# Kernel optimization log

Measured on AMD Instinct MI355X. Metric: run time of the kernel, lower is better.

Reference implementation:

```python
import jax, jax.numpy as jnp
import numpy as np

N_NODES = 100000
N_EDGES = 1600000
F_IN = 128
HID = 128
N_CLASSES = 32
N_GRAPHS = 512


def _seg_mean(vals, idx, num_segments):
    s = jax.ops.segment_sum(vals, idx, num_segments=num_segments)
    cnt = jax.ops.segment_sum(jnp.ones((vals.shape[0],), vals.dtype), idx, num_segments=num_segments)
    return s / jnp.maximum(cnt, 1.0)[:, None]


def _sage_conv(x, src, dst, Wl, bl, Wr):
    # PyG SAGEConv(mean): out = lin_l(mean_{j in N(i)} x_j) + lin_r(x_i); lin_l has bias, lin_r does not.
    agg = _seg_mean(x[src], dst, N_NODES)          # gather + scatter-mean  [N, d]
    return agg @ Wl.T + bl + x @ Wr.T              # [N, H]


def setup_inputs() -> dict:
    key = jax.random.key(0)
    ks = jax.random.split(key, 16)
    x = jax.random.normal(ks[0], (N_NODES, F_IN), dtype=jnp.float32)
    edge_index = jax.random.randint(ks[1], (2, N_EDGES), 0, N_NODES, dtype=jnp.int64)
    batch = jnp.sort(jax.random.randint(ks[2], (N_NODES,), 0, N_GRAPHS, dtype=jnp.int64))
    sc = 0.05
    params = {
        'Wl0': jax.random.normal(ks[3], (HID, F_IN), jnp.float32) * sc,
        'bl0': jnp.zeros((HID,), jnp.float32),
        'Wr0': jax.random.normal(ks[4], (HID, F_IN), jnp.float32) * sc,
        'Wl1': jax.random.normal(ks[5], (HID, HID), jnp.float32) * sc,
        'bl1': jnp.zeros((HID,), jnp.float32),
        'Wr1': jax.random.normal(ks[6], (HID, HID), jnp.float32) * sc,
        'Wl2': jax.random.normal(ks[7], (HID, HID), jnp.float32) * sc,
        'bl2': jnp.zeros((HID,), jnp.float32),
        'Wr2': jax.random.normal(ks[8], (HID, HID), jnp.float32) * sc,
        'Wlin': jax.random.normal(ks[9], (N_CLASSES, HID), jnp.float32) * sc,
        'blin': jnp.zeros((N_CLASSES,), jnp.float32),
    }
    return {'x': x, 'edge_index': edge_index, 'batch': batch, **params}


def reference(x, edge_index, batch, Wl0, bl0, Wr0, Wl1, bl1, Wr1, Wl2, bl2, Wr2, Wlin, blin):
    src, dst = edge_index[0], edge_index[1]
    # GraphSAGE backbone: relu between layers, no act after last (out_channels set); dropout=identity in eval.
    h = jax.nn.relu(_sage_conv(x, src, dst, Wl0, bl0, Wr0))
    h = jax.nn.relu(_sage_conv(h, src, dst, Wl1, bl1, Wr1))
    h = _sage_conv(h, src, dst, Wl2, bl2, Wr2)
    # global_mean_pool over batch index -> [n_graphs, HID]
    g = _seg_mean(h, batch, N_GRAPHS)
    return g @ Wlin.T + blin  # [n_graphs, n_classes]
```

## Files before the change

kernel.cpp:

```cpp
#include <hip/hip_runtime.h>
#include <hip/hip_bf16.h>


typedef __attribute__((ext_vector_type(8))) short short8v;
typedef __attribute__((ext_vector_type(4))) float f32x4;

#define RK_CH 12544
#define RK_NS 64

__device__ __forceinline__ unsigned short f2bf(float f) {
    __hip_bfloat16 h = __float2bfloat16(f);
    return *reinterpret_cast<unsigned short*>(&h);
}
__device__ __forceinline__ float bf_lo(unsigned u) { return __uint_as_float(u << 16); }
__device__ __forceinline__ float bf_hi(unsigned u) { return __uint_as_float(u & 0xffff0000u); }
__device__ __forceinline__ unsigned packbf(float lo, float hi) {
    return ((unsigned)f2bf(hi) << 16) | f2bf(lo);
}


__launch_bounds__(256)
__global__ void rank_hist_kernel(const int* __restrict__ dst,
                                 unsigned short* __restrict__ rank16,
                                 unsigned short* __restrict__ counts16,
                                 int nE, int nChunk, int es) {
    __shared__ unsigned cnt[RK_CH];
    int s = blockIdx.x / nChunk;
    int c = blockIdx.x % nChunk;
    int lo = c * RK_CH;
    for (int i = threadIdx.x; i < RK_CH; i += 256) cnt[i] = 0u;
    __syncthreads();

    int ebeg = s * es;
    int eend = ebeg + es; if (eend > nE) eend = nE;

    if (ebeg < eend) {
        if ((((size_t)dst) & 15) == 0) {
            int nvec = (eend - ebeg) >> 2;
            for (int g = threadIdx.x; g < nvec; g += 256) {
                int e = ebeg + g * 4;
                int4 d4 = *(const int4*)&dst[e];
                unsigned dc;
                dc = (unsigned)(d4.x - lo);
                if (dc < RK_CH) rank16[e]     = (unsigned short)atomicAdd(&cnt[dc], 1u);
                dc = (unsigned)(d4.y - lo);
                if (dc < RK_CH) rank16[e + 1] = (unsigned short)atomicAdd(&cnt[dc], 1u);
                dc = (unsigned)(d4.z - lo);
                if (dc < RK_CH) rank16[e + 2] = (unsigned short)atomicAdd(&cnt[dc], 1u);
                dc = (unsigned)(d4.w - lo);
                if (dc < RK_CH) rank16[e + 3] = (unsigned short)atomicAdd(&cnt[dc], 1u);
            }
            for (int e = ebeg + (nvec << 2) + threadIdx.x; e < eend; e += 256) {
                unsigned dc = (unsigned)(dst[e] - lo);
                if (dc < RK_CH) rank16[e] = (unsigned short)atomicAdd(&cnt[dc], 1u);
            }
        } else {
            for (int e = ebeg + threadIdx.x; e < eend; e += 256) {
                unsigned dc = (unsigned)(dst[e] - lo);
                if (dc < RK_CH) rank16[e] = (unsigned short)atomicAdd(&cnt[dc], 1u);
            }
        }
    }
    __syncthreads();
    size_t base = ((size_t)(c * RK_NS + s)) * RK_CH;
    for (int i = threadIdx.x; i < RK_CH; i += 256)
        counts16[base + i] = (unsigned short)cnt[i];
}

__global__ void seg_offsets_kernel(unsigned short* __restrict__ counts16,
                                   int* __restrict__ deg, int n) {
    int d = blockIdx.x * blockDim.x + threadIdx.x;
    if (d >= n) return;
    int c = d / RK_CH;
    int i = d - c * RK_CH;
    size_t base = ((size_t)c * RK_NS) * RK_CH + i;
    unsigned run = 0;
    for (int s = 0; s < RK_NS; ++s) {
        size_t idx = base + (size_t)s * RK_CH;
        unsigned v = counts16[idx];
        counts16[idx] = (unsigned short)run;
        run += v;
    }
    deg[d] = (int)run;
}

__global__ void scan1_kernel(const int* __restrict__ deg, int* __restrict__ rowptr,
                             int* __restrict__ bsum, int n) {
    __shared__ int s[1024];
    int lid = threadIdx.x;
    int i = blockIdx.x * 1024 + lid;
    int v = (i < n) ? deg[i] : 0;
    s[lid] = v;
    __syncthreads();
    #pragma unroll
    for (int off = 1; off < 1024; off <<= 1) {
        int t = (lid >= off) ? s[lid - off] : 0;
        __syncthreads();
        s[lid] += t;
        __syncthreads();
    }
    if (i < n) rowptr[i] = s[lid] - v;
    if (lid == 0) bsum[blockIdx.x] = s[1023];
}

__global__ void scan2_kernel(int* __restrict__ bsum, int nb) {
    __shared__ int s[1024];
    int lid = threadIdx.x;
    int v = (lid < nb) ? bsum[lid] : 0;
    s[lid] = v;
    __syncthreads();
    #pragma unroll
    for (int off = 1; off < 1024; off <<= 1) {
        int t = (lid >= off) ? s[lid - off] : 0;
        __syncthreads();
        s[lid] += t;
        __syncthreads();
    }
    if (lid < nb) bsum[lid] = s[lid] - v;
}

__global__ void scan3_kernel(int* __restrict__ rowptr, const int* __restrict__ bsum,
                             int n, int nE) {
    int i = blockIdx.x * blockDim.x + threadIdx.x;
    if (i < n) rowptr[i] += bsum[i >> 10];
    if (i == 0) rowptr[n] = nE;
}

__global__ void scatter2_kernel(const int* __restrict__ src, const int* __restrict__ dst,
                                const unsigned short* __restrict__ rank16,
                                const unsigned short* __restrict__ counts16,
                                const int* __restrict__ rowptr,
                                int* __restrict__ esrc, int nE, int es) {
    int e = blockIdx.x * blockDim.x + threadIdx.x;
    if (e >= nE) return;
    int d = dst[e];
    int s = e / es;
    int c = d / RK_CH;
    int i = d - c * RK_CH;
    int pos = rowptr[d] + (int)counts16[((size_t)(c * RK_NS + s)) * RK_CH + i]
                        + (int)rank16[e];
    esrc[pos] = src[e];
}


__global__ void cvt_kernel(const float* __restrict__ in, unsigned short* __restrict__ out, int n4) {
    int i = blockIdx.x * blockDim.x + threadIdx.x;
    if (i < n4) {
        float4 v = ((const float4*)in)[i];
        ushort4 o;
        o.x = f2bf(v.x); o.y = f2bf(v.y); o.z = f2bf(v.z); o.w = f2bf(v.w);
        ((ushort4*)out)[i] = o;
    }
}

__global__ void cvt6_kernel(const float* __restrict__ w0, const float* __restrict__ w1,
                            const float* __restrict__ w2, const float* __restrict__ w3,
                            const float* __restrict__ w4, const float* __restrict__ w5,
                            unsigned short* __restrict__ o0, unsigned short* __restrict__ o1,
                            unsigned short* __restrict__ o2, unsigned short* __restrict__ o3,
                            unsigned short* __restrict__ o4, unsigned short* __restrict__ o5,
                            int n4) {
    const float* in; unsigned short* out;
    switch (blockIdx.y) {
        case 0: in = w0; out = o0; break;
        case 1: in = w1; out = o1; break;
        case 2: in = w2; out = o2; break;
        case 3: in = w3; out = o3; break;
        case 4: in = w4; out = o4; break;
        default: in = w5; out = o5; break;
    }
    int i = blockIdx.x * blockDim.x + threadIdx.x;
    if (i < n4) {
        float4 v = ((const float4*)in)[i];
        ushort4 o;
        o.x = f2bf(v.x); o.y = f2bf(v.y); o.z = f2bf(v.z); o.w = f2bf(v.w);
        ((ushort4*)out)[i] = o;
    }
}


#define ACC8(v) do { \
    s0 += bf_lo((v).x); s1 += bf_hi((v).x); s2 += bf_lo((v).y); s3 += bf_hi((v).y); \
    s4 += bf_lo((v).z); s5 += bf_hi((v).z); s6 += bf_lo((v).w); s7 += bf_hi((v).w); } while (0)

__global__ void aggregate_kernel(const unsigned short* __restrict__ h,
                                 const int* __restrict__ rowptr,
                                 const int* __restrict__ esrc,
                                 unsigned short* __restrict__ agg, int n) {
    int wave = (blockIdx.x * blockDim.x + threadIdx.x) >> 6;
    int lane = threadIdx.x & 63;
    int q    = lane >> 4;
    int li   = lane & 15;
    int c0   = li * 8;
    int node = wave * 4 + q;

    int beg = 0, end = 0;
    if (node < n) { beg = rowptr[node]; end = rowptr[node + 1]; }

    float s0=0.f,s1=0.f,s2=0.f,s3=0.f,s4=0.f,s5=0.f,s6=0.f,s7=0.f;
    int j = beg;
    for (; j + 4 <= end; j += 4) {
        int r0 = esrc[j], r1 = esrc[j + 1], r2 = esrc[j + 2], r3 = esrc[j + 3];
        uint4 v0 = *(const uint4*)&h[(size_t)r0 * 128 + c0];
        uint4 v1 = *(const uint4*)&h[(size_t)r1 * 128 + c0];
        uint4 v2 = *(const uint4*)&h[(size_t)r2 * 128 + c0];
        uint4 v3 = *(const uint4*)&h[(size_t)r3 * 128 + c0];
        ACC8(v0); ACC8(v1); ACC8(v2); ACC8(v3);
    }
    for (; j < end; ++j) {
        int r0 = esrc[j];
        uint4 v0 = *(const uint4*)&h[(size_t)r0 * 128 + c0];
        ACC8(v0);
    }
    if (node < n) {
        int cnt = end - beg;
        float inv = 1.0f / (float)(cnt > 1 ? cnt : 1);
        uint4 o;
        o.x = packbf(s0 * inv, s1 * inv);
        o.y = packbf(s2 * inv, s3 * inv);
        o.z = packbf(s4 * inv, s5 * inv);
        o.w = packbf(s6 * inv, s7 * inv);
        *(uint4*)&agg[(size_t)node * 128 + c0] = o;
    }
}


__launch_bounds__(256)
__global__ void sage_gemm_mfma(const unsigned short* __restrict__ A,
                               const unsigned short* __restrict__ H,
                               const unsigned short* __restrict__ Wl,
                               const unsigned short* __restrict__ Wr,
                               const float* __restrict__ bl,
                               unsigned short* __restrict__ out, int n, int relu) {
    int tid  = threadIdx.x;
    int lane = tid & 63;
    int w    = tid >> 6;
    int wm   = w >> 1, wn = w & 1;
    int br   = blockIdx.x * 128 + wm * 64;
    int bc   = wn * 64;
    int lrow = lane & 15;
    int lk   = (lane >> 4) * 8;

    f32x4 acc[4][4] = {};

    #pragma unroll
    for (int half = 0; half < 2; ++half) {
        const unsigned short* X = half ? H : A;
        const unsigned short* W = half ? Wr : Wl;
        const unsigned short* xp[4];
        const unsigned short* wp[4];
        #pragma unroll
        for (int mb = 0; mb < 4; ++mb) {
            int r = br + mb * 16 + lrow;
            if (r >= n) r = n - 1;
            xp[mb] = X + (size_t)r * 128 + lk;
        }
        #pragma unroll
        for (int nb = 0; nb < 4; ++nb)
            wp[nb] = W + (size_t)(bc + nb * 16 + lrow) * 128 + lk;

        #pragma unroll
        for (int ks = 0; ks < 4; ++ks) {
            short8v a[4], b[4];
            #pragma unroll
            for (int mb = 0; mb < 4; ++mb) a[mb] = *(const short8v*)(xp[mb] + ks * 32);
            #pragma unroll
            for (int nb = 0; nb < 4; ++nb) b[nb] = *(const short8v*)(wp[nb] + ks * 32);
            #pragma unroll
            for (int mb = 0; mb < 4; ++mb)
                #pragma unroll
                for (int nb = 0; nb < 4; ++nb)
                    acc[mb][nb] = __builtin_amdgcn_mfma_f32_16x16x32_bf16(
                        a[mb], b[nb], acc[mb][nb], 0, 0, 0);
        }
    }

    int ccol  = lane & 15;
    int crow4 = (lane >> 4) * 4;
    float bv[4];
    #pragma unroll
    for (int nb = 0; nb < 4; ++nb) bv[nb] = bl[bc + nb * 16 + ccol];

    #pragma unroll
    for (int mb = 0; mb < 4; ++mb) {
        #pragma unroll
        for (int r = 0; r < 4; ++r) {
            int row = br + mb * 16 + crow4 + r;
            if (row < n) {
                #pragma unroll
                for (int nb = 0; nb < 4; ++nb) {
                    int col = bc + nb * 16 + ccol;
                    float v = acc[mb][nb][r] + bv[nb];
                    if (relu && v < 0.f) v = 0.f;
                    out[(size_t)row * 128 + col] = f2bf(v);
                }
            }
        }
    }
}


__device__ __forceinline__ int lbound(const int* __restrict__ a, int n, int v) {
    int lo = 0, hi = n;
    while (lo < hi) { int m = (lo + hi) >> 1; if (a[m] < v) lo = m + 1; else hi = m; }
    return lo;
}

__launch_bounds__(1024)
__global__ void pool_kernel(const unsigned short* __restrict__ h, const int* __restrict__ batch,
                            float* __restrict__ g, int n) {
    __shared__ float red[16][128];
    int b  = blockIdx.x;
    int rg = threadIdx.x >> 6;
    int cp = threadIdx.x & 63;
    int lo = lbound(batch, n, b);
    int hi = lbound(batch, n, b + 1);
    float s0 = 0.f, s1 = 0.f;
    for (int i = lo + rg; i < hi; i += 16) {
        unsigned v = *(const unsigned*)&h[(size_t)i * 128 + cp * 2];
        s0 += bf_lo(v); s1 += bf_hi(v);
    }
    red[rg][cp * 2]     = s0;
    red[rg][cp * 2 + 1] = s1;
    __syncthreads();
    #pragma unroll
    for (int off = 8; off >= 1; off >>= 1) {
        if (rg < off) {
            red[rg][cp * 2]     += red[rg + off][cp * 2];
            red[rg][cp * 2 + 1] += red[rg + off][cp * 2 + 1];
        }
        __syncthreads();
    }
    if (rg == 0) {
        int cnt = hi - lo;
        float inv = 1.0f / (float)(cnt > 1 ? cnt : 1);
        g[(size_t)b * 128 + cp * 2]     = red[0][cp * 2] * inv;
        g[(size_t)b * 128 + cp * 2 + 1] = red[0][cp * 2 + 1] * inv;
    }
}

__global__ void final_kernel(const float* __restrict__ g, const float* __restrict__ Wlin,
                             const float* __restrict__ blin, float* __restrict__ out, int total) {
    int gid = blockIdx.x * blockDim.x + threadIdx.x;
    if (gid >= total) return;
    int b = gid >> 5;
    int j = gid & 31;
    const float* gr = &g[(size_t)b * 128];
    const float* wr = &Wlin[(size_t)j * 128];
    float s = blin[j];
    #pragma unroll 4
    for (int c = 0; c < 128; ++c) s += gr[c] * wr[c];
    out[gid] = s;
}

extern "C" void kernel_launch(void* const* d_in, const int* in_sizes, int n_in,
                              void* d_out, int out_size, void* d_ws, size_t ws_size,
                              hipStream_t stream) {
    const float* x      = (const float*)d_in[0];
    const int*   eidx   = (const int*)d_in[1];
    const int*   batch  = (const int*)d_in[2];
    const float* Wl[3]  = {(const float*)d_in[3], (const float*)d_in[6], (const float*)d_in[9]};
    const float* bl[3]  = {(const float*)d_in[4], (const float*)d_in[7], (const float*)d_in[10]};
    const float* Wr[3]  = {(const float*)d_in[5], (const float*)d_in[8], (const float*)d_in[11]};
    const float* Wlin   = (const float*)d_in[12];
    const float* blin   = (const float*)d_in[13];
    float* out = (float*)d_out;

    const int N = in_sizes[0] / 128;
    const int E = in_sizes[1] / 2;
    const int G = out_size / 32;

    const int* esrc_in = eidx;
    const int* edst_in = eidx + E;

    char* w = (char*)d_ws;
    auto carve = [&](size_t bytes) { char* p = w; w += (bytes + 255) & ~(size_t)255; return p; };
    unsigned short* xbf  = (unsigned short*)carve((size_t)N * 128 * 2);
    unsigned short* hA   = (unsigned short*)carve((size_t)N * 128 * 2);
    unsigned short* hB   = (unsigned short*)carve((size_t)N * 128 * 2);
    unsigned short* agg  = (unsigned short*)carve((size_t)N * 128 * 2);
    unsigned short* Wbf[6];
    for (int i = 0; i < 6; ++i) Wbf[i] = (unsigned short*)carve((size_t)128 * 128 * 2);
    float* g      = (float*)carve((size_t)G * 128 * 4);
    int*   deg    = (int*)carve((size_t)N * 4);
    int*   rowptr = (int*)carve((size_t)(N + 1) * 4);
    int*   bsum   = (int*)carve(1024 * 4);
    int*   esrc   = (int*)carve((size_t)E * 4);
    unsigned short* rank16   = (unsigned short*)carve((size_t)E * 2);
    int nChunk = (N + RK_CH - 1) / RK_CH;
    unsigned short* counts16 = (unsigned short*)carve((size_t)nChunk * RK_NS * RK_CH * 2);
    (void)ws_size; (void)n_in;

    int es = (((E + RK_NS - 1) / RK_NS) + 3) & ~3;
    hipLaunchKernelGGL(rank_hist_kernel, dim3(nChunk * RK_NS), dim3(256), 0, stream,
                       edst_in, rank16, counts16, E, nChunk, es);
    int ngrid = (N + 255) / 256;
    hipLaunchKernelGGL(seg_offsets_kernel, dim3(ngrid), dim3(256), 0, stream,
                       counts16, deg, N);
    int nchunks = (N + 1023) / 1024;
    hipLaunchKernelGGL(scan1_kernel, dim3(nchunks), dim3(1024), 0, stream, deg, rowptr, bsum, N);
    hipLaunchKernelGGL(scan2_kernel, dim3(1), dim3(1024), 0, stream, bsum, nchunks);
    hipLaunchKernelGGL(scan3_kernel, dim3(ngrid), dim3(256), 0, stream, rowptr, bsum, N, E);
    int egrid = (E + 255) / 256;
    hipLaunchKernelGGL(scatter2_kernel, dim3(egrid), dim3(256), 0, stream,
                       esrc_in, edst_in, rank16, counts16, rowptr, esrc, E, es);

    int x4 = N * 128 / 4;
    hipLaunchKernelGGL(cvt_kernel, dim3((x4 + 255) / 256), dim3(256), 0, stream, x, xbf, x4);
    int w4 = 128 * 128 / 4;
    hipLaunchKernelGGL(cvt6_kernel, dim3((w4 + 255) / 256, 6), dim3(256), 0, stream,
                       Wl[0], Wr[0], Wl[1], Wr[1], Wl[2], Wr[2],
                       Wbf[0], Wbf[1], Wbf[2], Wbf[3], Wbf[4], Wbf[5], w4);

    int agrid = (N + 15) / 16;
    int ggrid = (N + 127) / 128;
    const unsigned short* hin = xbf;
    unsigned short* houts[3] = {hA, hB, hA};
    for (int l = 0; l < 3; ++l) {
        hipLaunchKernelGGL(aggregate_kernel, dim3(agrid), dim3(256), 0, stream,
                           hin, rowptr, esrc, agg, N);
        hipLaunchKernelGGL(sage_gemm_mfma, dim3(ggrid), dim3(256), 0, stream,
                           agg, hin, Wbf[2*l], Wbf[2*l+1], bl[l], houts[l], N, (l < 2) ? 1 : 0);
        hin = houts[l];
    }

    hipLaunchKernelGGL(pool_kernel, dim3(G), dim3(1024), 0, stream, hin, batch, g, N);
    int fgrid = (out_size + 255) / 256;
    hipLaunchKernelGGL(final_kernel, dim3(fgrid), dim3(256), 0, stream, g, Wlin, blin, out, out_size);
}
```

Measured before the change: 391.7 us.

## Restructure CSR scatter to process one dst-chunk per block over an edge slice

The edge scatter now launches one block per (dst chunk, edge slice) pair. Each block scans its whole slice with vectorized int4 loads and writes only the edges whose destination falls in its chunk. This keeps the counts16 row and the rowptr range per block localized in cache and confines the esrc writes to a chunk-sized region, in place of random global lookups per edge. In exchange, every edge slice is read once per chunk (8 chunks), which multiplies the reads of dst, src and rank16.

```diff
diff --git a/kernel.cpp b/kernel.cpp
--- a/kernel.cpp
+++ b/kernel.cpp
@@ -126,20 +126,40 @@
     if (i == 0) rowptr[n] = nE;
 }
 
-__global__ void scatter2_kernel(const int* __restrict__ src, const int* __restrict__ dst,
+__launch_bounds__(256)
+__global__ void scatter3_kernel(const int* __restrict__ src, const int* __restrict__ dst,
                                 const unsigned short* __restrict__ rank16,
                                 const unsigned short* __restrict__ counts16,
                                 const int* __restrict__ rowptr,
-                                int* __restrict__ esrc, int nE, int es) {
-    int e = blockIdx.x * blockDim.x + threadIdx.x;
-    if (e >= nE) return;
-    int d = dst[e];
-    int s = e / es;
-    int c = d / RK_CH;
-    int i = d - c * RK_CH;
-    int pos = rowptr[d] + (int)counts16[((size_t)(c * RK_NS + s)) * RK_CH + i]
-                        + (int)rank16[e];
-    esrc[pos] = src[e];
+                                int* __restrict__ esrc, int nE, int nChunk, int cpad, int es) {
+    int c = blockIdx.x % cpad;
+    int s = blockIdx.x / cpad;
+    if (c >= nChunk) return;
+    int lo = c * RK_CH;
+    const unsigned short* ctab = counts16 + ((size_t)(c * RK_NS + s)) * RK_CH;
+    int ebeg = s * es;
+    int eend = ebeg + es; if (eend > nE) eend = nE;
+    if (ebeg >= eend) return;
+    int nvec = (eend - ebeg) >> 2;
+    for (int g = threadIdx.x; g < nvec; g += 256) {
+        int e = ebeg + g * 4;
+        int4 d4 = *(const int4*)&dst[e];
+        int4 s4 = *(const int4*)&src[e];
+        ushort4 r4 = *(const ushort4*)&rank16[e];
+        unsigned dc;
+        dc = (unsigned)(d4.x - lo);
+        if (dc < RK_CH) esrc[rowptr[lo + dc] + (int)ctab[dc] + (int)r4.x] = s4.x;
+        dc = (unsigned)(d4.y - lo);
+        if (dc < RK_CH) esrc[rowptr[lo + dc] + (int)ctab[dc] + (int)r4.y] = s4.y;
+        dc = (unsigned)(d4.z - lo);
+        if (dc < RK_CH) esrc[rowptr[lo + dc] + (int)ctab[dc] + (int)r4.z] = s4.z;
+        dc = (unsigned)(d4.w - lo);
+        if (dc < RK_CH) esrc[rowptr[lo + dc] + (int)ctab[dc] + (int)r4.w] = s4.w;
+    }
+    for (int e = ebeg + (nvec << 2) + threadIdx.x; e < eend; e += 256) {
+        unsigned dc = (unsigned)(dst[e] - lo);
+        if (dc < RK_CH) esrc[rowptr[lo + dc] + (int)ctab[dc] + (int)rank16[e]] = src[e];
+    }
 }
 
 
@@ -401,9 +421,9 @@
     hipLaunchKernelGGL(scan1_kernel, dim3(nchunks), dim3(1024), 0, stream, deg, rowptr, bsum, N);
     hipLaunchKernelGGL(scan2_kernel, dim3(1), dim3(1024), 0, stream, bsum, nchunks);
     hipLaunchKernelGGL(scan3_kernel, dim3(ngrid), dim3(256), 0, stream, rowptr, bsum, N, E);
-    int egrid = (E + 255) / 256;
-    hipLaunchKernelGGL(scatter2_kernel, dim3(egrid), dim3(256), 0, stream,
-                       esrc_in, edst_in, rank16, counts16, rowptr, esrc, E, es);
+    int cpad = (nChunk + 7) & ~7;
+    hipLaunchKernelGGL(scatter3_kernel, dim3(RK_NS * cpad), dim3(256), 0, stream,
+                       esrc_in, edst_in, rank16, counts16, rowptr, esrc, E, nChunk, cpad, es);
 
     int x4 = N * 128 / 4;
     hipLaunchKernelGGL(cvt_kernel, dim3((x4 + 255) / 256), dim3(256), 0, stream, x, xbf, x4);
```

After: 406.3 us. 1.04x slower.

## Fuse preprocessing, segment-offset/scan, and pool/head kernels to cut launches

Applied to the files above, without the earlier changes.

Merges the rank histogram, x conversion and weight conversion into one heterogeneous-grid kernel, so the conversions can overlap the histogram. Folds the per-node segment-offset pass into the first scan kernel, which drops the deg buffer. Fuses global mean pooling with the final linear head. This removes several launches and intermediate round-trips, but the fused scan does its strided count walk in 1024-thread blocks, and the non-aligned fallback in the histogram path is dropped.

```diff
diff --git a/kernel.cpp b/kernel.cpp
--- a/kernel.cpp
+++ b/kernel.cpp
@@ -20,22 +20,33 @@
 
 
 __launch_bounds__(256)
-__global__ void rank_hist_kernel(const int* __restrict__ dst,
-                                 unsigned short* __restrict__ rank16,
-                                 unsigned short* __restrict__ counts16,
-                                 int nE, int nChunk, int es) {
+__global__ void pre_kernel(const int* __restrict__ dst,
+                           unsigned short* __restrict__ rank16,
+                           unsigned short* __restrict__ counts16,
+                           int nE, int nChunk, int es,
+                           const float* __restrict__ x, unsigned short* __restrict__ xbf, int x4,
+                           const float* __restrict__ w0, const float* __restrict__ w1,
+                           const float* __restrict__ w2, const float* __restrict__ w3,
+                           const float* __restrict__ w4, const float* __restrict__ w5,
+                           unsigned short* __restrict__ o0, unsigned short* __restrict__ o1,
+                           unsigned short* __restrict__ o2, unsigned short* __restrict__ o3,
+                           unsigned short* __restrict__ o4, unsigned short* __restrict__ o5,
+                           int w4n, int w4b) {
     __shared__ unsigned cnt[RK_CH];
-    int s = blockIdx.x / nChunk;
-    int c = blockIdx.x % nChunk;
-    int lo = c * RK_CH;
-    for (int i = threadIdx.x; i < RK_CH; i += 256) cnt[i] = 0u;
-    __syncthreads();
-
-    int ebeg = s * es;
-    int eend = ebeg + es; if (eend > nE) eend = nE;
-
-    if (ebeg < eend) {
-        if ((((size_t)dst) & 15) == 0) {
+    int rhB  = nChunk * RK_NS;
+    int cvtB = (x4 + 255) / 256;
+    int bid  = blockIdx.x;
+
+    if (bid < rhB) {
+        int s = bid / nChunk;
+        int c = bid % nChunk;
+        int lo = c * RK_CH;
+        for (int i = threadIdx.x; i < RK_CH; i += 256) cnt[i] = 0u;
+        __syncthreads();
+
+        int ebeg = s * es;
+        int eend = ebeg + es; if (eend > nE) eend = nE;
+        if (ebeg < eend) {
             int nvec = (eend - ebeg) >> 2;
             for (int g = threadIdx.x; g < nvec; g += 256) {
                 int e = ebeg + g * 4;
@@ -54,42 +65,63 @@
                 unsigned dc = (unsigned)(dst[e] - lo);
                 if (dc < RK_CH) rank16[e] = (unsigned short)atomicAdd(&cnt[dc], 1u);
             }
-        } else {
-            for (int e = ebeg + threadIdx.x; e < eend; e += 256) {
-                unsigned dc = (unsigned)(dst[e] - lo);
-                if (dc < RK_CH) rank16[e] = (unsigned short)atomicAdd(&cnt[dc], 1u);
-            }
-        }
-    }
-    __syncthreads();
-    size_t base = ((size_t)(c * RK_NS + s)) * RK_CH;
-    for (int i = threadIdx.x; i < RK_CH; i += 256)
-        counts16[base + i] = (unsigned short)cnt[i];
-}
-
-__global__ void seg_offsets_kernel(unsigned short* __restrict__ counts16,
-                                   int* __restrict__ deg, int n) {
-    int d = blockIdx.x * blockDim.x + threadIdx.x;
-    if (d >= n) return;
-    int c = d / RK_CH;
-    int i = d - c * RK_CH;
-    size_t base = ((size_t)c * RK_NS) * RK_CH + i;
-    unsigned run = 0;
-    for (int s = 0; s < RK_NS; ++s) {
-        size_t idx = base + (size_t)s * RK_CH;
-        unsigned v = counts16[idx];
-        counts16[idx] = (unsigned short)run;
-        run += v;
-    }
-    deg[d] = (int)run;
-}
-
-__global__ void scan1_kernel(const int* __restrict__ deg, int* __restrict__ rowptr,
-                             int* __restrict__ bsum, int n) {
+        }
+        __syncthreads();
+        size_t base = ((size_t)(c * RK_NS + s)) * RK_CH;
+        for (int i = threadIdx.x; i < RK_CH; i += 256)
+            counts16[base + i] = (unsigned short)cnt[i];
+    } else if (bid < rhB + cvtB) {
+        int i = (bid - rhB) * 256 + threadIdx.x;
+        if (i < x4) {
+            float4 v = ((const float4*)x)[i];
+            ushort4 o;
+            o.x = f2bf(v.x); o.y = f2bf(v.y); o.z = f2bf(v.z); o.w = f2bf(v.w);
+            ((ushort4*)xbf)[i] = o;
+        }
+    } else {
+        int idx  = bid - rhB - cvtB;
+        int wsel = idx / w4b;
+        int wb   = idx % w4b;
+        const float* in; unsigned short* out;
+        switch (wsel) {
+            case 0: in = w0; out = o0; break;
+            case 1: in = w1; out = o1; break;
+            case 2: in = w2; out = o2; break;
+            case 3: in = w3; out = o3; break;
+            case 4: in = w4; out = o4; break;
+            default: in = w5; out = o5; break;
+        }
+        int i = wb * 256 + threadIdx.x;
+        if (i < w4n) {
+            float4 v = ((const float4*)in)[i];
+            ushort4 o;
+            o.x = f2bf(v.x); o.y = f2bf(v.y); o.z = f2bf(v.z); o.w = f2bf(v.w);
+            ((ushort4*)out)[i] = o;
+        }
+    }
+}
+
+
+__launch_bounds__(1024)
+__global__ void seg_scan1_kernel(unsigned short* __restrict__ counts16,
+                                 int* __restrict__ rowptr, int* __restrict__ bsum, int n) {
     __shared__ int s[1024];
     int lid = threadIdx.x;
-    int i = blockIdx.x * 1024 + lid;
-    int v = (i < n) ? deg[i] : 0;
+    int d = blockIdx.x * 1024 + lid;
+    int v = 0;
+    if (d < n) {
+        int c = d / RK_CH;
+        int i = d - c * RK_CH;
+        size_t base = ((size_t)c * RK_NS) * RK_CH + i;
+        unsigned run = 0;
+        for (int sl = 0; sl < RK_NS; ++sl) {
+            size_t idx = base + (size_t)sl * RK_CH;
+            unsigned t = counts16[idx];
+            counts16[idx] = (unsigned short)run;
+            run += t;
+        }
+        v = (int)run;
+    }
     s[lid] = v;
     __syncthreads();
     #pragma unroll
@@ -99,7 +131,7 @@
         s[lid] += t;
         __syncthreads();
     }
-    if (i < n) rowptr[i] = s[lid] - v;
+    if (d < n) rowptr[d] = s[lid] - v;
     if (lid == 0) bsum[blockIdx.x] = s[1023];
 }
 
@@ -140,42 +172,6 @@
     int pos = rowptr[d] + (int)counts16[((size_t)(c * RK_NS + s)) * RK_CH + i]
                         + (int)rank16[e];
     esrc[pos] = src[e];
-}
-
-
-__global__ void cvt_kernel(const float* __restrict__ in, unsigned short* __restrict__ out, int n4) {
-    int i = blockIdx.x * blockDim.x + threadIdx.x;
-    if (i < n4) {
-        float4 v = ((const float4*)in)[i];
-        ushort4 o;
-        o.x = f2bf(v.x); o.y = f2bf(v.y); o.z = f2bf(v.z); o.w = f2bf(v.w);
-        ((ushort4*)out)[i] = o;
-    }
-}
-
-__global__ void cvt6_kernel(const float* __restrict__ w0, const float* __restrict__ w1,
-                            const float* __restrict__ w2, const float* __restrict__ w3,
-                            const float* __restrict__ w4, const float* __restrict__ w5,
-                            unsigned short* __restrict__ o0, unsigned short* __restrict__ o1,
-                            unsigned short* __restrict__ o2, unsigned short* __restrict__ o3,
-                            unsigned short* __restrict__ o4, unsigned short* __restrict__ o5,
-                            int n4) {
-    const float* in; unsigned short* out;
-    switch (blockIdx.y) {
-        case 0: in = w0; out = o0; break;
-        case 1: in = w1; out = o1; break;
-        case 2: in = w2; out = o2; break;
-        case 3: in = w3; out = o3; break;
-        case 4: in = w4; out = o4; break;
-        default: in = w5; out = o5; break;
-    }
-    int i = blockIdx.x * blockDim.x + threadIdx.x;
-    if (i < n4) {
-        float4 v = ((const float4*)in)[i];
-        ushort4 o;
-        o.x = f2bf(v.x); o.y = f2bf(v.y); o.z = f2bf(v.z); o.w = f2bf(v.w);
-        ((ushort4*)out)[i] = o;
-    }
 }
 
 
@@ -307,8 +303,11 @@
 }
 
 __launch_bounds__(1024)
-__global__ void pool_kernel(const unsigned short* __restrict__ h, const int* __restrict__ batch,
-                            float* __restrict__ g, int n) {
+__global__ void pool_head_kernel(const unsigned short* __restrict__ h,
+                                 const int* __restrict__ batch,
+                                 const float* __restrict__ Wlin,
+                                 const float* __restrict__ blin,
+                                 float* __restrict__ out, int n) {
     __shared__ float red[16][128];
     int b  = blockIdx.x;
     int rg = threadIdx.x >> 6;
@@ -331,26 +330,16 @@
         }
         __syncthreads();
     }
-    if (rg == 0) {
+    if (threadIdx.x < 32) {
+        int j = threadIdx.x;
         int cnt = hi - lo;
         float inv = 1.0f / (float)(cnt > 1 ? cnt : 1);
-        g[(size_t)b * 128 + cp * 2]     = red[0][cp * 2] * inv;
-        g[(size_t)b * 128 + cp * 2 + 1] = red[0][cp * 2 + 1] * inv;
-    }
-}
-
-__global__ void final_kernel(const float* __restrict__ g, const float* __restrict__ Wlin,
-                             const float* __restrict__ blin, float* __restrict__ out, int total) {
-    int gid = blockIdx.x * blockDim.x + threadIdx.x;
-    if (gid >= total) return;
-    int b = gid >> 5;
-    int j = gid & 31;
-    const float* gr = &g[(size_t)b * 128];
-    const float* wr = &Wlin[(size_t)j * 128];
-    float s = blin[j];
-    #pragma unroll 4
-    for (int c = 0; c < 128; ++c) s += gr[c] * wr[c];
-    out[gid] = s;
+        const float* wr = &Wlin[(size_t)j * 128];
+        float s = 0.f;
+        #pragma unroll 4
+        for (int c = 0; c < 128; ++c) s += red[0][c] * wr[c];
+        out[(size_t)b * 32 + j] = blin[j] + s * inv;
+    }
 }
 
 extern "C" void kernel_launch(void* const* d_in, const int* in_sizes, int n_in,
@@ -368,7 +357,6 @@
 
     const int N = in_sizes[0] / 128;
     const int E = in_sizes[1] / 2;
-    const int G = out_size / 32;
 
     const int* esrc_in = eidx;
     const int* edst_in = eidx + E;
@@ -381,8 +369,6 @@
     unsigned short* agg  = (unsigned short*)carve((size_t)N * 128 * 2);
     unsigned short* Wbf[6];
     for (int i = 0; i < 6; ++i) Wbf[i] = (unsigned short*)carve((size_t)128 * 128 * 2);
-    float* g      = (float*)carve((size_t)G * 128 * 4);
-    int*   deg    = (int*)carve((size_t)N * 4);
     int*   rowptr = (int*)carve((size_t)(N + 1) * 4);
     int*   bsum   = (int*)carve(1024 * 4);
     int*   esrc   = (int*)carve((size_t)E * 4);
@@ -392,25 +378,27 @@
     (void)ws_size; (void)n_in;
 
     int es = (((E + RK_NS - 1) / RK_NS) + 3) & ~3;
-    hipLaunchKernelGGL(rank_hist_kernel, dim3(nChunk * RK_NS), dim3(256), 0, stream,
-                       edst_in, rank16, counts16, E, nChunk, es);
+    int x4   = N * 128 / 4;
+    int cvtB = (x4 + 255) / 256;
+    int w4n  = 128 * 128 / 4;
+    int w4b  = (w4n + 255) / 256;
+    int rhB  = nChunk * RK_NS;
+    hipLaunchKernelGGL(pre_kernel, dim3(rhB + cvtB + 6 * w4b), dim3(256), 0, stream,
+                       edst_in, rank16, counts16, E, nChunk, es,
+                       x, xbf, x4,
+                       Wl[0], Wr[0], Wl[1], Wr[1], Wl[2], Wr[2],
+                       Wbf[0], Wbf[1], Wbf[2], Wbf[3], Wbf[4], Wbf[5],
+                       w4n, w4b);
+
+    int nchunks = (N + 1023) / 1024;
+    hipLaunchKernelGGL(seg_scan1_kernel, dim3(nchunks), dim3(1024), 0, stream,
+                       counts16, rowptr, bsum, N);
+    hipLaunchKernelGGL(scan2_kernel, dim3(1), dim3(1024), 0, stream, bsum, nchunks);
     int ngrid = (N + 255) / 256;
-    hipLaunchKernelGGL(seg_offsets_kernel, dim3(ngrid), dim3(256), 0, stream,
-                       counts16, deg, N);
-    int nchunks = (N + 1023) / 1024;
-    hipLaunchKernelGGL(scan1_kernel, dim3(nchunks), dim3(1024), 0, stream, deg, rowptr, bsum, N);
-    hipLaunchKernelGGL(scan2_kernel, dim3(1), dim3(1024), 0, stream, bsum, nchunks);
     hipLaunchKernelGGL(scan3_kernel, dim3(ngrid), dim3(256), 0, stream, rowptr, bsum, N, E);
     int egrid = (E + 255) / 256;
     hipLaunchKernelGGL(scatter2_kernel, dim3(egrid), dim3(256), 0, stream,
                        esrc_in, edst_in, rank16, counts16, rowptr, esrc, E, es);
-
-    int x4 = N * 128 / 4;
-    hipLaunchKernelGGL(cvt_kernel, dim3((x4 + 255) / 256), dim3(256), 0, stream, x, xbf, x4);
-    int w4 = 128 * 128 / 4;
-    hipLaunchKernelGGL(cvt6_kernel, dim3((w4 + 255) / 256, 6), dim3(256), 0, stream,
-                       Wl[0], Wr[0], Wl[1], Wr[1], Wl[2], Wr[2],
-                       Wbf[0], Wbf[1], Wbf[2], Wbf[3], Wbf[4], Wbf[5], w4);
 
     int agrid = (N + 15) / 16;
     int ggrid = (N + 127) / 128;
@@ -424,7 +412,7 @@
         hin = houts[l];
     }
 
-    hipLaunchKernelGGL(pool_kernel, dim3(G), dim3(1024), 0, stream, hin, batch, g, N);
-    int fgrid = (out_size + 255) / 256;
-    hipLaunchKernelGGL(final_kernel, dim3(fgrid), dim3(256), 0, stream, g, Wlin, blin, out, out_size);
-}
+    int G = out_size / 32;
+    hipLaunchKernelGGL(pool_head_kernel, dim3(G), dim3(1024), 0, stream,
+                       hin, batch, Wlin, blin, out, N);
+}
```

Measured after the change: 383.0 us (median of 2 runs). -2.2%, faster.
